# Optimization experiments

Measured on AMD Instinct MI355X. Metric: run time of the kernel, lower is better.

## Reference

```python
import jax, jax.numpy as jnp
import numpy as np

DIM = 384
NH = 6
HD = DIM // NH  # 64
WS = (6, 12)    # window_size (dilated_size=[1,1] so total_window_size == window_size)
SS = (3, 6)     # shift_size
N = WS[0] * WS[1]  # 72 tokens per window


def _make_mask(H, W):
    # Faithful replication of SD_attn.create_mask (static, so computed in numpy).
    wh, ww = WS
    sh, sw = SS
    img = np.zeros((H, W), np.float32)
    cnt = 0
    for hs in (slice(0, -wh), slice(-wh, -sh), slice(-sh, None)):
        for wsl in (slice(0, -ww), slice(-ww, 0), slice(0, None)):
            img[hs, wsl] = cnt
            cnt += 1
    # window partition -> (nW, N)
    m = img.reshape(H // wh, wh, W // ww, ww).transpose(0, 2, 1, 3).reshape(-1, wh * ww)
    d = m[:, None, :] - m[:, :, None]  # (nW, N, N), [i,j] = m[j]-m[i]
    return np.where(d != 0, -np.inf, 0.0).astype(np.float32)


def _rope2d(x):
    # 2D axial rotary embedding over the (wh, ww) window grid.
    # x: (M, wh, ww, hd); first half of pair-channels rotated by h-position, second half by w-position.
    wh, ww, hd = x.shape[1], x.shape[2], x.shape[3]
    half = hd // 2
    inv = 1.0 / (10000.0 ** (np.arange(0, half, 2, dtype=np.float32) / half))  # (half//2,)
    ah = np.arange(wh, dtype=np.float32)[:, None] * inv  # (wh, half//2)
    aw = np.arange(ww, dtype=np.float32)[:, None] * inv  # (ww, half//2)
    ang = np.concatenate([
        np.broadcast_to(ah[:, None, :], (wh, ww, half // 2)),
        np.broadcast_to(aw[None, :, :], (wh, ww, half // 2)),
    ], -1)  # (wh, ww, half)
    cos = jnp.asarray(np.cos(ang), dtype=x.dtype)
    sin = jnp.asarray(np.sin(ang), dtype=x.dtype)
    x1, x2 = x[..., 0::2], x[..., 1::2]
    return jnp.stack([x1 * cos - x2 * sin, x1 * sin + x2 * cos], -1).reshape(x.shape)


def setup_inputs() -> dict:
    key = jax.random.key(0)
    ks = jax.random.split(key, 5)
    x = jax.random.normal(ks[0], (2, 192, 384, DIM), jnp.float32)
    w_qkv = 0.02 * jax.random.normal(ks[1], (3 * DIM, DIM), jnp.float32)
    b_qkv = 0.02 * jax.random.normal(ks[2], (3 * DIM,), jnp.float32)
    w_proj = 0.02 * jax.random.normal(ks[3], (DIM, DIM), jnp.float32)
    b_proj = 0.02 * jax.random.normal(ks[4], (DIM,), jnp.float32)
    return {"x": x, "w_qkv": w_qkv, "b_qkv": b_qkv, "w_proj": w_proj, "b_proj": b_proj}


def reference(x, w_qkv, b_qkv, w_proj, b_proj):
    B, H, W, C = x.shape
    wh, ww = WS
    sh, sw = SS
    nH, nWc = H // wh, W // ww
    nwin = nH * nWc
    B_ = B * nwin
    scale = HD ** -0.5

    # cyclic shift + window partition (dilated_size=[1,1] => plain swin windows)
    xs = jnp.roll(x, (-sh, -sw), axis=(1, 2))
    xw = xs.reshape(B, nH, wh, nWc, ww, C).transpose(0, 1, 3, 2, 4, 5).reshape(B_, N, C)

    qkv = (xw @ w_qkv.T + b_qkv).reshape(B_, N, 3, NH, HD).transpose(2, 0, 3, 1, 4)
    q, k, v = qkv[0], qkv[1], qkv[2]  # (B_, NH, N, HD)

    q = _rope2d(q.reshape(-1, wh, ww, HD)).reshape(B_, NH, N, HD)
    k = _rope2d(k.reshape(-1, wh, ww, HD)).reshape(B_, NH, N, HD)

    attn = jnp.einsum('bhnd,bhmd->bhnm', q * scale, k)  # (B_, NH, N, N)
    mask = jnp.asarray(_make_mask(H, W))                 # (nwin, N, N)
    attn = (attn.reshape(B, nwin, NH, N, N) + mask[None, :, None]).reshape(B_, NH, N, N)
    attn = jax.nn.softmax(attn, axis=-1)
    save_attn = attn.mean(axis=1)  # mean over heads -> (B_, N, N)

    out = jnp.einsum('bhnm,bhmd->bhnd', attn, v).transpose(0, 2, 1, 3).reshape(B_, N, C)
    out = out.reshape(B, nH, nWc, wh, ww, C).transpose(0, 1, 3, 2, 4, 5).reshape(B, H, W, C)
    out = jnp.roll(out, (sh, sw), axis=(1, 2))
    out = out @ w_proj.T + b_proj
    return out, save_attn
```

## Files before the change

### kernel.cpp

```cpp
#include <hip/hip_runtime.h>

typedef __attribute__((ext_vector_type(8))) __bf16 bf16x8;
typedef __attribute__((ext_vector_type(4))) float f32x4;
typedef unsigned short u16;
typedef unsigned int u32;

__device__ __forceinline__ u16 f2bf(float x){
  u32 u = __float_as_uint(x);
  return (u16)((u + 0x7fffu + ((u >> 16) & 1u)) >> 16);
}
__device__ __forceinline__ u32 pkbf(float lo, float hi){
  u32 r; asm("v_cvt_pk_bf16_f32 %0, %1, %2" : "=v"(r) : "v"(lo), "v"(hi)); return r;
}

union FragU { uint4 u4; bf16x8 bf; };

__device__ __forceinline__ bf16x8 lds_frag(const unsigned char* smem, int off, int row, int strideB, int kElem){
  int byte = (row * strideB + kElem * 2) ^ ((row & 7) << 4);
  FragU f; f.u4 = *reinterpret_cast<const uint4*>(smem + off + byte);
  return f.bf;
}

typedef __attribute__((address_space(3))) unsigned char lds_u8;
typedef __attribute__((address_space(1))) const unsigned char g_u8;
__device__ __forceinline__ void glds16(const void* g, void* l){
  __builtin_amdgcn_global_load_lds((g_u8*)g, (lds_u8*)l, 16, 0, 0);
}

__global__ void prep_weights(const float* __restrict__ wq, const float* __restrict__ wp,
                             u16* __restrict__ wqb, u16* __restrict__ wpb){
  int i = blockIdx.x * 256 + threadIdx.x;
  wqb[i] = f2bf(wq[i]);
  if (i < 147456) wpb[i] = f2bf(wp[i]);
}

__global__ void prep_x(const float* __restrict__ x, u16* __restrict__ xb){
  size_t i = ((size_t)blockIdx.x * 256 + threadIdx.x) * 8;
  float4 f0 = *reinterpret_cast<const float4*>(x + i);
  float4 f1 = *reinterpret_cast<const float4*>(x + i + 4);
  uint4 q;
  q.x = pkbf(f0.x, f0.y); q.y = pkbf(f0.z, f0.w);
  q.z = pkbf(f1.x, f1.y); q.w = pkbf(f1.z, f1.w);
  *reinterpret_cast<uint4*>(xb + i) = q;
}

#define WA_OFF 0
#define WB_OFF 10240
#define WVT    0
#define WTC    61440
#define WTS    62592
__launch_bounds__(256, 2)
__global__ void qkv_win(const u16* __restrict__ xb, const u16* __restrict__ wqb,
                        const float* __restrict__ bq, float* __restrict__ out,
                        u16* __restrict__ vws)
{
  __shared__ __align__(16) unsigned char smem[63744];
  const int tid  = threadIdx.x;
  const int wc   = tid >> 6;
  const int lane = tid & 63;
  const int l15  = lane & 15;
  const int lhi  = lane >> 4;

  const int bid = blockIdx.x;
  const int l   = (bid & 7) * 768 + (bid >> 3);
  const int g   = l / 3;
  const int sec = l - g * 3;
  const int bIdx = g >> 10;
  const int win  = g & 1023;
  const int wi   = win >> 5;
  const int wj   = win & 31;

  auto rowof = [&](int t)->size_t {
    int r = t / 12, c = t - r * 12;
    int hh = wi * 6 + r + 3;  if (hh >= 192) hh -= 192;
    int ww = wj * 12 + c + 6; if (ww >= 384) ww -= 384;
    return ((size_t)bIdx * 192 + hh) * 384 + ww;
  };

  float* tabc = reinterpret_cast<float*>(smem + WTC);
  float* tabs = reinterpret_cast<float*>(smem + WTS);
  for (int i = tid; i < 288; i += 256){
    int pos = i >> 4, m = i & 15;
    float pv = (pos < 6) ? (float)pos : (float)(pos - 6);
    float ang = pv * __expf(-(float)m * 0.5756462732485114f);
    tabc[i] = cosf(ang);
    tabs[i] = sinf(ang);
  }

  size_t arow[3]; int asoff[3]; bool aval[3];
  #pragma unroll
  for (int it = 0; it < 3; ++it){
    int c = it * 256 + tid;
    aval[it] = (it < 2) || (tid < 128);
    int t = c >> 3, p = c & 7;
    int tc = (t < 72) ? t : 71;
    arow[it]  = rowof(tc);
    asoff[it] = ((p ^ (t & 7)) << 3);
  }

  f32x4 acc[5][6];
  #pragma unroll
  for (int mt = 0; mt < 5; ++mt)
    #pragma unroll
    for (int nt = 0; nt < 6; ++nt) acc[mt][nt] = 0.0f;

  for (int kk = 0; kk < 6; ++kk){
    #pragma unroll
    for (int it = 0; it < 3; ++it){
      if (aval[it])
        glds16(xb + arow[it] * 384 + kk * 64 + asoff[it],
               smem + WA_OFF + (it * 256 + tid) * 16);
    }
    #pragma unroll
    for (int it = 0; it < 12; ++it){
      int c = it * 256 + tid;
      int n = c >> 3, p = c & 7;
      glds16(wqb + (size_t)(sec * 384 + n) * 384 + kk * 64 + ((p ^ (n & 7)) << 3),
             smem + WB_OFF + c * 16);
    }
    __syncthreads();
    #pragma unroll
    for (int ks = 0; ks < 2; ++ks){
      const int kEl = ks * 32 + lhi * 8;
      bf16x8 af[5], bfr[6];
      #pragma unroll
      for (int mt = 0; mt < 5; ++mt)
        af[mt] = lds_frag(smem, WA_OFF, mt * 16 + l15, 128, kEl);
      #pragma unroll
      for (int nt = 0; nt < 6; ++nt)
        bfr[nt] = lds_frag(smem, WB_OFF, wc * 96 + nt * 16 + l15, 128, kEl);
      __builtin_amdgcn_s_setprio(1);
      #pragma unroll
      for (int mt = 0; mt < 5; ++mt)
        #pragma unroll
        for (int nt = 0; nt < 6; ++nt)
          acc[mt][nt] = __builtin_amdgcn_mfma_f32_16x16x32_bf16(af[mt], bfr[nt], acc[mt][nt], 0, 0, 0);
      __builtin_amdgcn_s_setprio(0);
    }
    __syncthreads();
  }

  if (sec < 2){
    u16* qk = (u16*)out + (sec ? 56623104u : 0u) + (size_t)g * 27648;
    #pragma unroll
    for (int nt = 0; nt < 6; ++nt){
      const int ch  = wc * 96 + nt * 16 + l15;
      const int h   = ch >> 6;
      const int chh = ch & 63;
      const float bias = bq[sec * 384 + ch];
      const int p2  = chh >> 1;
      const int m   = p2 & 15;
      const bool isR = (p2 < 16);
      const bool ev  = ((chh & 1) == 0);
      #pragma unroll
      for (int mt = 0; mt < 5; ++mt){
        #pragma unroll
        for (int r = 0; r < 4; ++r){
          const int tok = mt * 16 + lhi * 4 + r;
          float v = acc[mt][nt][r] + bias;
          float o = __shfl_xor(v, 1);
          int tr = tok / 12;
          int pos = isR ? tr : (6 + tok - tr * 12);
          float cc = tabc[pos * 16 + m], ssn = tabs[pos * 16 + m];
          float nv = ev ? (v * cc - o * ssn) : (o * ssn + v * cc);
          if (sec == 0) nv *= 0.125f;
          if (tok < 72)
            qk[(size_t)h * 4608 + tok * 64 + chh] = f2bf(nv);
        }
      }
    }
  } else {
    #pragma unroll
    for (int nt = 0; nt < 6; ++nt){
      const int ch = wc * 96 + nt * 16 + l15;
      const float bv = bq[768 + ch];
      #pragma unroll
      for (int mt = 0; mt < 5; ++mt){
        const int tok0 = mt * 16 + lhi * 4;
        uint2 pk;
        pk.x = pkbf(acc[mt][nt][0] + bv, acc[mt][nt][1] + bv);
        pk.y = pkbf(acc[mt][nt][2] + bv, acc[mt][nt][3] + bv);
        *reinterpret_cast<uint2*>(smem + WVT + ch * 160 + tok0 * 2) = pk;
      }
    }
    __syncthreads();
    u16* vd = vws + (size_t)g * 30720;
    #pragma unroll
    for (int it = 0; it < 15; ++it){
      int c  = it * 256 + tid;
      int ch = c / 10;
      int p  = c - ch * 10;
      uint4 val;
      if (p == 9){ val.x = 0; val.y = 0; val.z = 0; val.w = 0; }
      else val = *reinterpret_cast<const uint4*>(smem + WVT + c * 16);
      *reinterpret_cast<uint4*>(vd + (size_t)(ch >> 6) * 5120 + (ch & 63) * 80 + p * 8) = val;
    }
  }
}

#define QH4 0
#define KH4 10240
#define VT4 20480
#define SMEM4 30976
__launch_bounds__(320, 5)
__global__ void win_attn6(const u16* __restrict__ qkg,
                          const u16* __restrict__ vws,
                          float* __restrict__ out,
                          u16* __restrict__ axb)
{
  __shared__ __align__(16) unsigned char smem[SMEM4];
  const int tid  = threadIdx.x;
  const int wave = tid >> 6;
  const int lane = tid & 63;
  const int l15  = lane & 15;
  const int lhi  = lane >> 4;

  const int bid  = blockIdx.x;
  const int wgid = (bid & 7) * 256 + (bid >> 3);
  const int bIdx = wgid >> 10;
  const int win  = wgid & 1023;
  const int wi   = win >> 5;
  const int wj   = win & 31;
  const bool maskWin = (wi == 31);
  const int g    = wgid;

  auto rowof = [&](int t)->size_t {
    int r = t / 12, c = t - r * 12;
    int hh = wi * 6 + r + 3;  if (hh >= 192) hh -= 192;
    int ww = wj * 12 + c + 6; if (ww >= 384) ww -= 384;
    return ((size_t)bIdx * 192 + hh) * 384 + ww;
  };
  const int qtok = wave * 16 + l15;
  const bool tv = (qtok < 72);
  const size_t qrow = rowof(tv ? qtok : 71);

  const u16* qsl0 = qkg + (size_t)g * 27648;
  const u16* ksl0 = qkg + 56623104u + (size_t)g * 27648;
  const u16* vsl0 = vws + (size_t)g * 30720;

  if (tid < 64) *reinterpret_cast<u32*>(smem + VT4 + 10240 + tid * 4) = 0u;

  float sv[5][4];
  #pragma unroll
  for (int a2 = 0; a2 < 5; ++a2)
    #pragma unroll
    for (int b2 = 0; b2 < 4; ++b2) sv[a2][b2] = 0.0f;

  for (int h = 0; h < 6; ++h){
    const u16* qsl = qsl0 + h * 4608;
    const u16* ksl = ksl0 + h * 4608;
    const u16* vsl = vsl0 + h * 5120;
    #pragma unroll
    for (int it = 0; it < 2; ++it){
      int c = it * 320 + tid;
      int t = c >> 3, p = c & 7;
      int tc = (t < 72) ? t : 71;
      int s = (p ^ (t & 7)) << 3;
      glds16(qsl + tc * 64 + s, smem + QH4 + c * 16);
      glds16(ksl + tc * 64 + s, smem + KH4 + c * 16);
      glds16(vsl + c * 8,       smem + VT4 + c * 16);
    }
    __syncthreads();

    f32x4 pf[5];
    #pragma unroll
    for (int nt = 0; nt < 5; ++nt) pf[nt] = 0.0f;
    __builtin_amdgcn_s_setprio(1);
    #pragma unroll
    for (int ks = 0; ks < 2; ++ks){
      const int kEl = ks * 32 + lhi * 8;
      bf16x8 qf = lds_frag(smem, QH4, qtok, 128, kEl);
      #pragma unroll
      for (int nt = 0; nt < 5; ++nt){
        bf16x8 kf = lds_frag(smem, KH4, nt * 16 + l15, 128, kEl);
        pf[nt] = __builtin_amdgcn_mfma_f32_16x16x32_bf16(kf, qf, pf[nt], 0, 0, 0);
      }
    }
    __builtin_amdgcn_s_setprio(0);

    float mx = -1e30f;
    #pragma unroll
    for (int nt = 0; nt < 5; ++nt)
      #pragma unroll
      for (int r = 0; r < 4; ++r){
        const int kk2 = nt * 16 + lhi * 4 + r;
        bool valid = (kk2 < 72) && (!maskWin || ((kk2 < 36) == (qtok < 36)));
        float val = valid ? pf[nt][r] : -1e30f;
        pf[nt][r] = val;
        mx = fmaxf(mx, val);
      }
    mx = fmaxf(mx, __shfl_xor(mx, 16));
    mx = fmaxf(mx, __shfl_xor(mx, 32));
    float sm = 0.0f;
    #pragma unroll
    for (int nt = 0; nt < 5; ++nt)
      #pragma unroll
      for (int r = 0; r < 4; ++r){
        float e = __expf(pf[nt][r] - mx);
        pf[nt][r] = e; sm += e;
      }
    sm += __shfl_xor(sm, 16);
    sm += __shfl_xor(sm, 32);
    const float inv = 1.0f / sm;
    u32 pp[5][2];
    #pragma unroll
    for (int nt = 0; nt < 5; ++nt){
      float p0 = pf[nt][0] * inv, p1 = pf[nt][1] * inv;
      float p2 = pf[nt][2] * inv, p3 = pf[nt][3] * inv;
      sv[nt][0] += p0; sv[nt][1] += p1; sv[nt][2] += p2; sv[nt][3] += p3;
      pp[nt][0] = pkbf(p0, p1);
      pp[nt][1] = pkbf(p2, p3);
    }

    f32x4 oacc[4];
    #pragma unroll
    for (int nt = 0; nt < 4; ++nt) oacc[nt] = 0.0f;
    #pragma unroll
    for (int ks = 0; ks < 3; ++ks){
      FragU pb;
      u32 w[4];
      #pragma unroll
      for (int w_ = 0; w_ < 4; ++w_){
        int srcLane = l15 + 16 * ((lane >> 4 & 1) * 2 + (w_ >> 1));
        u32 c0 = __shfl(pp[ks * 2][w_ & 1], srcLane);
        u32 c1 = (ks * 2 + 1 < 5) ? __shfl(pp[ks * 2 + 1][w_ & 1], srcLane) : 0u;
        w[w_] = (lhi & 2) ? c1 : c0;
      }
      pb.u4.x = w[0]; pb.u4.y = w[1]; pb.u4.z = w[2]; pb.u4.w = w[3];
      const int kEl = ks * 32 + lhi * 8;
      __builtin_amdgcn_s_setprio(1);
      #pragma unroll
      for (int nt = 0; nt < 4; ++nt){
        FragU vf;
        vf.u4 = *reinterpret_cast<const uint4*>(smem + VT4 + (nt * 16 + l15) * 160 + kEl * 2);
        oacc[nt] = __builtin_amdgcn_mfma_f32_16x16x32_bf16(vf.bf, pb.bf, oacc[nt], 0, 0, 0);
      }
      __builtin_amdgcn_s_setprio(0);
    }
    if (tv){
      u16* ao = axb + qrow * 384 + h * 64;
      #pragma unroll
      for (int nt = 0; nt < 4; ++nt){
        uint2 pk;
        pk.x = pkbf(oacc[nt][0], oacc[nt][1]);
        pk.y = pkbf(oacc[nt][2], oacc[nt][3]);
        *reinterpret_cast<uint2*>(ao + nt * 16 + lhi * 4) = pk;
      }
    }
    __syncthreads();
  }

  if (tv){
    float* so = out + 56623104ull + (size_t)wgid * 5184 + (size_t)qtok * 72;
    const float c6 = 1.0f / 6.0f;
    #pragma unroll
    for (int nt = 0; nt < 4; ++nt){
      float4 v4; v4.x = sv[nt][0]*c6; v4.y = sv[nt][1]*c6; v4.z = sv[nt][2]*c6; v4.w = sv[nt][3]*c6;
      *reinterpret_cast<float4*>(so + nt * 16 + lhi * 4) = v4;
    }
    if (lhi < 2){
      float4 v4; v4.x = sv[4][0]*c6; v4.y = sv[4][1]*c6; v4.z = sv[4][2]*c6; v4.w = sv[4][3]*c6;
      *reinterpret_cast<float4*>(so + 64 + lhi * 4) = v4;
    }
  }
}

#define B6STR 12288
__launch_bounds__(512, 4)
__global__ void proj_gemm2(const u16* __restrict__ axb,
                           const u16* __restrict__ wpb, const float* __restrict__ bp,
                           float* __restrict__ out)
{
  __shared__ __align__(16) unsigned char smem[24576];
  const int tid  = threadIdx.x;
  const int wave = tid >> 6;
  const int lane = tid & 63;
  const int l15  = lane & 15;
  const int lhi  = lane >> 4;
  const int wr   = wave >> 2;
  const int wc   = wave & 3;
  const size_t row0 = (size_t)blockIdx.x * 128;
  const int ny   = blockIdx.y;

  const u16* bsec = wpb + (size_t)(ny * 192) * 384;
  auto stageB = [&](int t, int bufOff){
    {
      int c = tid, row = c >> 2, ccd = c & 3;
      int ccs = ccd ^ ((row >> 1) & 3);
      glds16(bsec + (size_t)row * 384 + t * 32 + ccs * 8, smem + bufOff + c * 16);
    }
    if (tid < 256){
      int c = 512 + tid, row = c >> 2, ccd = c & 3;
      int ccs = ccd ^ ((row >> 1) & 3);
      glds16(bsec + (size_t)row * 384 + t * 32 + ccs * 8, smem + bufOff + c * 16);
    }
  };

  const u16* abase = axb + (row0 + wr * 64 + l15) * 384 + lhi * 8;

  f32x4 acc[4][3];
  #pragma unroll
  for (int mt = 0; mt < 4; ++mt)
    #pragma unroll
    for (int nt = 0; nt < 3; ++nt) acc[mt][nt] = 0.0f;

  FragU a_cur[4], a_nxt[4];
  #pragma unroll
  for (int mt = 0; mt < 4; ++mt)
    a_cur[mt].u4 = *reinterpret_cast<const uint4*>(abase + mt * 6144);
  stageB(0, 0);
  __syncthreads();

  int buf = 0;
  for (int t = 0; t < 12; ++t){
    if (t < 11){
      stageB(t + 1, buf ^ B6STR);
      #pragma unroll
      for (int mt = 0; mt < 4; ++mt)
        a_nxt[mt].u4 = *reinterpret_cast<const uint4*>(abase + mt * 6144 + (t + 1) * 32);
    }
    FragU bfr[3];
    #pragma unroll
    for (int nt = 0; nt < 3; ++nt){
      int rown = wc * 48 + nt * 16 + l15;
      int byte = buf + rown * 64 + ((lhi ^ ((rown >> 1) & 3)) << 4);
      bfr[nt].u4 = *reinterpret_cast<const uint4*>(smem + byte);
    }
    #pragma unroll
    for (int mt = 0; mt < 4; ++mt)
      #pragma unroll
      for (int nt = 0; nt < 3; ++nt)
        acc[mt][nt] = __builtin_amdgcn_mfma_f32_16x16x32_bf16(a_cur[mt].bf, bfr[nt].bf, acc[mt][nt], 0, 0, 0);
    __syncthreads();
    #pragma unroll
    for (int mt = 0; mt < 4; ++mt) a_cur[mt] = a_nxt[mt];
    buf ^= B6STR;
  }

  float bpv[3];
  #pragma unroll
  for (int nt = 0; nt < 3; ++nt) bpv[nt] = bp[ny * 192 + wc * 48 + nt * 16 + l15];
  #pragma unroll
  for (int mt = 0; mt < 4; ++mt)
    #pragma unroll
    for (int nt = 0; nt < 3; ++nt){
      const int ch = ny * 192 + wc * 48 + nt * 16 + l15;
      #pragma unroll
      for (int r = 0; r < 4; ++r){
        size_t grow = row0 + wr * 64 + mt * 16 + lhi * 4 + r;
        out[grow * 384 + ch] = acc[mt][nt][r] + bpv[nt];
      }
    }
}

extern "C" void kernel_launch(void* const* d_in, const int* in_sizes, int n_in,
                              void* d_out, int out_size, void* d_ws, size_t ws_size,
                              hipStream_t stream)
{
  const float* x  = (const float*)d_in[0];
  const float* wq = (const float*)d_in[1];
  const float* bq = (const float*)d_in[2];
  const float* wp = (const float*)d_in[3];
  const float* bp = (const float*)d_in[4];
  float* out = (float*)d_out;

  u16* wqb = (u16*)d_ws;
  u16* wpb = (u16*)((char*)d_ws + 442368 * 2);
  u16* vws = (u16*)((char*)d_ws + 1179648);
  u16* xb  = (u16*)((char*)d_ws + 127008768);

  prep_weights<<<1728, 256, 0, stream>>>(wq, wp, wqb, wpb);
  prep_x<<<27648, 256, 0, stream>>>(x, xb);
  qkv_win<<<6144, 256, 0, stream>>>(xb, wqb, bq, out, vws);
  win_attn6<<<2048, 320, 0, stream>>>((const u16*)out, vws, out, xb);
  proj_gemm2<<<dim3(1152, 2), 512, 0, stream>>>(xb, wpb, bp, out);
}
```

Measured before the change: 636.3 us.

## Fuse prep kernels, prefetch first QKV tile early, remap proj grid for XCD locality

```diff
diff --git a/kernel.cpp b/kernel.cpp
--- a/kernel.cpp
+++ b/kernel.cpp
@@ -27,21 +27,22 @@
   __builtin_amdgcn_global_load_lds((g_u8*)g, (lds_u8*)l, 16, 0, 0);
 }
 
-__global__ void prep_weights(const float* __restrict__ wq, const float* __restrict__ wp,
-                             u16* __restrict__ wqb, u16* __restrict__ wpb){
-  int i = blockIdx.x * 256 + threadIdx.x;
-  wqb[i] = f2bf(wq[i]);
-  if (i < 147456) wpb[i] = f2bf(wp[i]);
-}
-
-__global__ void prep_x(const float* __restrict__ x, u16* __restrict__ xb){
-  size_t i = ((size_t)blockIdx.x * 256 + threadIdx.x) * 8;
+__global__ void prep_all(const float* __restrict__ x, u16* __restrict__ xb,
+                         const float* __restrict__ wq, const float* __restrict__ wp,
+                         u16* __restrict__ wqb, u16* __restrict__ wpb){
+  const int bidx = blockIdx.x;
+  size_t i = ((size_t)bidx * 256 + threadIdx.x) * 8;
   float4 f0 = *reinterpret_cast<const float4*>(x + i);
   float4 f1 = *reinterpret_cast<const float4*>(x + i + 4);
   uint4 q;
   q.x = pkbf(f0.x, f0.y); q.y = pkbf(f0.z, f0.w);
   q.z = pkbf(f1.x, f1.y); q.w = pkbf(f1.z, f1.w);
   *reinterpret_cast<uint4*>(xb + i) = q;
+  if (bidx < 1728){
+    int j = bidx * 256 + threadIdx.x;
+    wqb[j] = f2bf(wq[j]);
+    if (j < 147456) wpb[j] = f2bf(wp[j]);
+  }
 }
 
 #define WA_OFF 0
@@ -77,6 +78,31 @@
     return ((size_t)bIdx * 192 + hh) * 384 + ww;
   };
 
+  size_t arow[3]; int asoff[3]; bool aval[3];
+  #pragma unroll
+  for (int it = 0; it < 3; ++it){
+    int c = it * 256 + tid;
+    aval[it] = (it < 2) || (tid < 128);
+    int t = c >> 3, p = c & 7;
+    int tc = (t < 72) ? t : 71;
+    arow[it]  = rowof(tc);
+    asoff[it] = ((p ^ (t & 7)) << 3);
+  }
+
+  #pragma unroll
+  for (int it = 0; it < 3; ++it){
+    if (aval[it])
+      glds16(xb + arow[it] * 384 + asoff[it],
+             smem + WA_OFF + (it * 256 + tid) * 16);
+  }
+  #pragma unroll
+  for (int it = 0; it < 12; ++it){
+    int c = it * 256 + tid;
+    int n = c >> 3, p = c & 7;
+    glds16(wqb + (size_t)(sec * 384 + n) * 384 + ((p ^ (n & 7)) << 3),
+           smem + WB_OFF + c * 16);
+  }
+
   float* tabc = reinterpret_cast<float*>(smem + WTC);
   float* tabs = reinterpret_cast<float*>(smem + WTS);
   for (int i = tid; i < 288; i += 256){
@@ -87,17 +113,6 @@
     tabs[i] = sinf(ang);
   }
 
-  size_t arow[3]; int asoff[3]; bool aval[3];
-  #pragma unroll
-  for (int it = 0; it < 3; ++it){
-    int c = it * 256 + tid;
-    aval[it] = (it < 2) || (tid < 128);
-    int t = c >> 3, p = c & 7;
-    int tc = (t < 72) ? t : 71;
-    arow[it]  = rowof(tc);
-    asoff[it] = ((p ^ (t & 7)) << 3);
-  }
-
   f32x4 acc[5][6];
   #pragma unroll
   for (int mt = 0; mt < 5; ++mt)
@@ -105,18 +120,20 @@
     for (int nt = 0; nt < 6; ++nt) acc[mt][nt] = 0.0f;
 
   for (int kk = 0; kk < 6; ++kk){
-    #pragma unroll
-    for (int it = 0; it < 3; ++it){
-      if (aval[it])
-        glds16(xb + arow[it] * 384 + kk * 64 + asoff[it],
-               smem + WA_OFF + (it * 256 + tid) * 16);
-    }
-    #pragma unroll
-    for (int it = 0; it < 12; ++it){
-      int c = it * 256 + tid;
-      int n = c >> 3, p = c & 7;
-      glds16(wqb + (size_t)(sec * 384 + n) * 384 + kk * 64 + ((p ^ (n & 7)) << 3),
-             smem + WB_OFF + c * 16);
+    if (kk > 0){
+      #pragma unroll
+      for (int it = 0; it < 3; ++it){
+        if (aval[it])
+          glds16(xb + arow[it] * 384 + kk * 64 + asoff[it],
+                 smem + WA_OFF + (it * 256 + tid) * 16);
+      }
+      #pragma unroll
+      for (int it = 0; it < 12; ++it){
+        int c = it * 256 + tid;
+        int n = c >> 3, p = c & 7;
+        glds16(wqb + (size_t)(sec * 384 + n) * 384 + kk * 64 + ((p ^ (n & 7)) << 3),
+               smem + WB_OFF + c * 16);
+      }
     }
     __syncthreads();
     #pragma unroll
@@ -379,8 +396,11 @@
   const int lhi  = lane >> 4;
   const int wr   = wave >> 2;
   const int wc   = wave & 3;
-  const size_t row0 = (size_t)blockIdx.x * 128;
-  const int ny   = blockIdx.y;
+
+  const int bid = blockIdx.x;
+  const int l   = (bid & 7) * 288 + (bid >> 3);
+  const size_t row0 = (size_t)(l >> 1) * 128;
+  const int ny  = l & 1;
 
   const u16* bsec = wpb + (size_t)(ny * 192) * 384;
   auto stageB = [&](int t, int bufOff){
@@ -469,9 +489,8 @@
   u16* vws = (u16*)((char*)d_ws + 1179648);
   u16* xb  = (u16*)((char*)d_ws + 127008768);
 
-  prep_weights<<<1728, 256, 0, stream>>>(wq, wp, wqb, wpb);
-  prep_x<<<27648, 256, 0, stream>>>(x, xb);
+  prep_all<<<27648, 256, 0, stream>>>(x, xb, wq, wp, wqb, wpb);
   qkv_win<<<6144, 256, 0, stream>>>(xb, wqb, bq, out, vws);
   win_attn6<<<2048, 320, 0, stream>>>((const u16*)out, vws, out, xb);
-  proj_gemm2<<<dim3(1152, 2), 512, 0, stream>>>(xb, wpb, bp, out);
-}
+  proj_gemm2<<<2304, 512, 0, stream>>>(xb, wpb, bp, out);
+}
```

After: 708.2 us. 1.11x slower.
